# Optimization experiments

Measured on AMD Instinct MI355X. Metric: run time of the kernel, lower is better.

## Reference

```python
import jax, jax.numpy as jnp
import numpy as np

B = 32        # events per batch
NP = 1024     # hits per event (in_hits)
K = 30        # kNN neighbors (includes self, as in PyG knn)
D_IN = 7      # hit feature dim (hardcoded SegmentationNet(7, ...))
OUT = 2       # out_channels


def _edge_conv(x, W1, b1, s, t, W2, b2, k):
    """DynamicEdgeConv: x [B,n,d] -> [B,n,64].
    kNN in feature space, edge MLP on [x_i, x_j - x_i], max-aggregate.
    BN (eval mode) folded into per-channel scale s and shift t."""
    sq = jnp.sum(x * x, axis=-1)                           # [B,n]
    d2 = sq[:, :, None] + sq[:, None, :] - 2.0 * jnp.einsum('bnd,bmd->bnm', x, x)
    _, idx = jax.lax.top_k(-d2, k)                         # [B,n,k] nearest (self included)
    xj = jax.vmap(lambda xb, ib: xb[ib])(x, idx)           # [B,n,k,d] gather neighbors
    xi = jnp.broadcast_to(x[:, :, None, :], xj.shape)
    e = jnp.concatenate([xi, xj - xi], axis=-1)            # [B,n,k,2d]
    h = jax.nn.relu((e @ W1 + b1) * s + t)                 # Linear + BN(eval) + ReLU
    h = h @ W2 + b2                                        # plain last layer (PyG MLP)
    return jnp.max(h, axis=2)                              # max aggregation over k


def setup_inputs() -> dict:
    key = jax.random.key(0)
    ks = jax.random.split(key, 40)
    def lin(k, fi, fo):
        return jax.random.normal(k, (fi, fo), jnp.float32) / np.float32(np.sqrt(fi))
    def vec(k, n, scale=0.1):
        return jax.random.normal(k, (n,), jnp.float32) * np.float32(scale)
    inp = {}
    inp['pos'] = jax.random.normal(ks[0], (B * NP, D_IN), jnp.float32)
    inp['batch'] = jnp.repeat(jnp.arange(B, dtype=jnp.int32), NP)
    inp['batch_size'] = B
    # conv1 edge MLP: [14,64] + BN + ReLU, [64,64]
    inp['c1_W1'] = lin(ks[1], 2 * D_IN, 64); inp['c1_b1'] = vec(ks[2], 64)
    inp['c1_s'] = 1.0 + vec(ks[3], 64); inp['c1_t'] = vec(ks[4], 64)
    inp['c1_W2'] = lin(ks[5], 64, 64); inp['c1_b2'] = vec(ks[6], 64)
    # conv2/conv3: [128,64] + BN + ReLU, [64,64]
    inp['c2_W1'] = lin(ks[7], 128, 64); inp['c2_b1'] = vec(ks[8], 64)
    inp['c2_s'] = 1.0 + vec(ks[9], 64); inp['c2_t'] = vec(ks[10], 64)
    inp['c2_W2'] = lin(ks[11], 64, 64); inp['c2_b2'] = vec(ks[12], 64)
    inp['c3_W1'] = lin(ks[13], 128, 64); inp['c3_b1'] = vec(ks[14], 64)
    inp['c3_s'] = 1.0 + vec(ks[15], 64); inp['c3_t'] = vec(ks[16], 64)
    inp['c3_W2'] = lin(ks[17], 64, 64); inp['c3_b2'] = vec(ks[18], 64)
    # segmentation head MLP [192,1024,256,128,OUT], norm=None, eval (dropout off)
    inp['h_W1'] = lin(ks[19], 192, 1024); inp['h_b1'] = vec(ks[20], 1024)
    inp['h_W2'] = lin(ks[21], 1024, 256); inp['h_b2'] = vec(ks[22], 256)
    inp['h_W3'] = lin(ks[23], 256, 128); inp['h_b3'] = vec(ks[24], 128)
    inp['h_W4'] = lin(ks[25], 128, OUT); inp['h_b4'] = vec(ks[26], OUT)
    # wrapper MLP: Linear(NP*OUT, 100), ReLU, Linear(100, OUT)
    inp['m_W1'] = lin(ks[27], NP * OUT, 100); inp['m_b1'] = vec(ks[28], 100)
    inp['m_W2'] = lin(ks[29], 100, OUT); inp['m_b2'] = vec(ks[30], OUT)
    return inp


def reference(pos, batch, batch_size,
              c1_W1, c1_b1, c1_s, c1_t, c1_W2, c1_b2,
              c2_W1, c2_b1, c2_s, c2_t, c2_W2, c2_b2,
              c3_W1, c3_b1, c3_s, c3_t, c3_W2, c3_b2,
              h_W1, h_b1, h_W2, h_b2, h_W3, h_b3, h_W4, h_b4,
              m_W1, m_b1, m_W2, m_b2):
    n = pos.shape[0] // batch_size
    x = pos.reshape(batch_size, n, -1)          # uniform contiguous graphs per `batch`
    x1 = _edge_conv(x, c1_W1, c1_b1, c1_s, c1_t, c1_W2, c1_b2, K)
    x2 = _edge_conv(x1, c2_W1, c2_b1, c2_s, c2_t, c2_W2, c2_b2, K)
    x3 = _edge_conv(x2, c3_W1, c3_b1, c3_s, c3_t, c3_W2, c3_b2, K)
    h = jnp.concatenate([x1, x2, x3], axis=-1)  # [B,n,192]
    h = jax.nn.relu(h @ h_W1 + h_b1)
    h = jax.nn.relu(h @ h_W2 + h_b2)
    h = jax.nn.relu(h @ h_W3 + h_b3)
    h = h @ h_W4 + h_b4
    seg = jax.nn.log_softmax(h, axis=-1)        # per-node log-probs [B,n,OUT]
    flat = seg.reshape(batch_size, -1)          # [B, n*OUT]
    y = jax.nn.relu(flat @ m_W1 + m_b1) @ m_W2 + m_b2
    return jax.nn.log_softmax(y, axis=-1)       # [B, OUT]
```

## Files before the change

kernel.cpp:

```cpp
#include <hip/hip_runtime.h>
#include <math.h>

#define NPB   1024
#define NB    32
#define NTOT  (NPB * NB)
#define KNN_K 30
#define QB    32
#define DSTR  1028
#define FINF  __builtin_inff()

typedef __attribute__((ext_vector_type(8))) short bf16x8;
typedef __attribute__((ext_vector_type(4))) float f32x4;
typedef unsigned short ushort_t;

__device__ inline ushort_t f2bf(float f) {
  unsigned u = __builtin_bit_cast(unsigned, f);
  u += 0x7FFFu + ((u >> 16) & 1u);
  return (ushort_t)(u >> 16);
}
__device__ inline float bf2f(ushort_t h) {
  return __builtin_bit_cast(float, (unsigned)h << 16);
}

__device__ __forceinline__ void select_row(const float* row, int jbase,
                                           int* out, unsigned* cb, int lane) {
  unsigned u[16];
  #pragma unroll
  for (int i = 0; i < 16; ++i) {
    const unsigned b = __builtin_bit_cast(unsigned, row[lane + (i << 6)]);
    u[i] = b ^ ((unsigned)((int)b >> 31) | 0x80000000u);
  }
  unsigned m = u[0];
  #pragma unroll
  for (int i = 1; i < 16; ++i) m = min(m, u[i]);
  #pragma unroll
  for (int k = 2; k <= 64; k <<= 1) {
    #pragma unroll
    for (int jj = k >> 1; jj >= 1; jj >>= 1) {
      const unsigned o = (unsigned)__shfl_xor((int)m, jj);
      const bool up    = ((lane & k) == 0);
      const bool lower = ((lane & jj) == 0);
      m = (lower == up) ? min(m, o) : max(m, o);
    }
  }
  const unsigned T = (unsigned)__shfl((int)m, 29);

  unsigned mask16 = 0; int cnt = 0;
  #pragma unroll
  for (int i = 0; i < 16; ++i) {
    const bool sv = (u[i] <= T);
    mask16 |= (sv ? 1u : 0u) << i;
    cnt += sv;
  }
  int sc = cnt;
  #pragma unroll
  for (int o = 1; o < 64; o <<= 1) {
    const int v = __shfl_up(sc, o);
    if (lane >= o) sc += v;
  }
  const int base = sc - cnt;
  const int tot  = __shfl(sc, 63);

  if (tot <= 128) {
    int p = base;
    #pragma unroll
    for (int i = 0; i < 16; ++i) {
      if ((mask16 >> i) & 1u)
        cb[p++] = (u[i] & 0xFFFFFC00u) | (unsigned)(lane + (i << 6));
    }
    for (int q = tot + lane; q < 128; q += 64) cb[q] = 0xFFFFFFFFu;
    unsigned r0 = cb[lane];
    unsigned r1 = cb[lane + 64];
    #pragma unroll
    for (int k = 2; k <= 128; k <<= 1) {
      #pragma unroll
      for (int jj = k >> 1; jj >= 1; jj >>= 1) {
        if (jj == 64) {
          const unsigned lo = min(r0, r1), hi = max(r0, r1);
          r0 = lo; r1 = hi;
        } else {
          const unsigned o0 = (unsigned)__shfl_xor((int)r0, jj);
          const unsigned o1 = (unsigned)__shfl_xor((int)r1, jj);
          const bool lower = ((lane & jj) == 0);
          const bool up0 = ((lane & k) == 0);
          const bool up1 = (((lane + 64) & k) == 0);
          r0 = (lower == up0) ? min(r0, o0) : max(r0, o0);
          r1 = (lower == up1) ? min(r1, o1) : max(r1, o1);
        }
      }
    }
    if (lane < KNN_K) out[lane] = jbase + (int)(r0 & 1023u);
  } else {
    unsigned pk[16];
    #pragma unroll
    for (int i = 0; i < 16; ++i)
      pk[i] = (u[i] & 0xFFFFFC00u) | (unsigned)(lane + (i << 6));
    #pragma unroll 1
    for (int k = 0; k < KNN_K; ++k) {
      unsigned best = pk[0];
      #pragma unroll
      for (int i = 1; i < 16; ++i) best = min(best, pk[i]);
      #pragma unroll
      for (int o = 32; o > 0; o >>= 1)
        best = min(best, (unsigned)__shfl_xor((int)best, o));
      if (lane == 0) out[k] = jbase + (int)(best & 1023u);
      #pragma unroll
      for (int i = 0; i < 16; ++i) if (pk[i] == best) pk[i] = 0xFFFFFFFFu;
    }
  }
}

__global__ __launch_bounds__(512)
void knn64_kernel(const ushort_t* __restrict__ X, int lda,
                  const float* __restrict__ sq, int* __restrict__ idx) {
  __shared__ float d2l[QB * DSTR];
  __shared__ float sqa[QB];
  __shared__ unsigned cbuf[8][128];
  const int tid = threadIdx.x;
  const int wave = tid >> 6, lane = tid & 63;
  const int g = lane >> 4, r16 = lane & 15;
  const int nbase = blockIdx.y * NPB;
  const int q0 = blockIdx.x * QB;
  if (tid < QB) sqa[tid] = sq[nbase + q0 + tid];
  __syncthreads();

  const int n0 = wave * 128;
  bf16x8 a0[2], a1[2];
  #pragma unroll
  for (int ks = 0; ks < 2; ++ks) {
    a0[ks] = *(const bf16x8*)(X + (size_t)(nbase + q0 + r16) * lda + ks * 32 + g * 8);
    a1[ks] = *(const bf16x8*)(X + (size_t)(nbase + q0 + 16 + r16) * lda + ks * 32 + g * 8);
  }
  #pragma unroll
  for (int nt = 0; nt < 8; ++nt) {
    const int col = n0 + nt * 16 + r16;
    f32x4 acc0 = (f32x4)(0.f), acc1 = (f32x4)(0.f);
    #pragma unroll
    for (int ks = 0; ks < 2; ++ks) {
      const bf16x8 b = *(const bf16x8*)(X + (size_t)(nbase + col) * lda + ks * 32 + g * 8);
      acc0 = __builtin_amdgcn_mfma_f32_16x16x32_bf16(a0[ks], b, acc0, 0, 0, 0);
      acc1 = __builtin_amdgcn_mfma_f32_16x16x32_bf16(a1[ks], b, acc1, 0, 0, 0);
    }
    const float sb = sq[nbase + col];
    #pragma unroll
    for (int r = 0; r < 4; ++r) {
      const int row0 = g * 4 + r;
      d2l[row0 * DSTR + col] = sqa[row0] + sb - 2.f * acc0[r];
      d2l[(16 + row0) * DSTR + col] = sqa[16 + row0] + sb - 2.f * acc1[r];
    }
  }
  __syncthreads();

  #pragma unroll 1
  for (int rr = 0; rr < 4; ++rr) {
    const int row = wave * 4 + rr;
    select_row(&d2l[row * DSTR], nbase,
               idx + (size_t)(nbase + q0 + row) * KNN_K, cbuf[wave], lane);
  }
}

__global__ __launch_bounds__(512)
void knn7_kernel(const float* __restrict__ pos,
                 const float* __restrict__ sq, int* __restrict__ idx) {
  __shared__ float d2l[QB * DSTR];
  __shared__ float Xq[QB][8];
  __shared__ float sqa[QB];
  __shared__ unsigned cbuf[8][128];
  const int tid = threadIdx.x;
  const int wave = tid >> 6, lane = tid & 63;
  const int nbase = blockIdx.y * NPB;
  const int q0 = blockIdx.x * QB;
  if (tid < QB * 8) {
    const int row = tid >> 3, d = tid & 7;
    Xq[row][d] = (d < 7) ? pos[(size_t)(nbase + q0 + row) * 7 + d] : 0.f;
  }
  if (tid >= 256 && tid < 256 + QB) sqa[tid - 256] = sq[nbase + q0 + tid - 256];
  __syncthreads();

  const int c0 = wave * 128 + lane;
  float xc0[7], xc1[7];
  #pragma unroll
  for (int d = 0; d < 7; ++d) {
    xc0[d] = pos[(size_t)(nbase + c0) * 7 + d];
    xc1[d] = pos[(size_t)(nbase + c0 + 64) * 7 + d];
  }
  const float sb0 = sq[nbase + c0], sb1 = sq[nbase + c0 + 64];
  #pragma unroll 1
  for (int row = 0; row < QB; ++row) {
    float q[7];
    #pragma unroll
    for (int d = 0; d < 7; ++d) q[d] = Xq[row][d];
    float d0 = 0.f, d1 = 0.f;
    #pragma unroll
    for (int d = 0; d < 7; ++d) { d0 += q[d] * xc0[d]; d1 += q[d] * xc1[d]; }
    const float sa = sqa[row];
    d2l[row * DSTR + c0]      = sa + sb0 - 2.f * d0;
    d2l[row * DSTR + c0 + 64] = sa + sb1 - 2.f * d1;
  }
  __syncthreads();

  #pragma unroll 1
  for (int rr = 0; rr < 4; ++rr) {
    const int row = wave * 4 + rr;
    select_row(&d2l[row * DSTR], nbase,
               idx + (size_t)(nbase + q0 + row) * KNN_K, cbuf[wave], lane);
  }
}

template<int D>
__global__ __launch_bounds__(256)
void sq_kernel(const float* __restrict__ x, int lda, float* __restrict__ sq) {
  const int wave = threadIdx.x >> 6, c = threadIdx.x & 63;
  const int nb = blockIdx.x * 16 + wave * 4;
  #pragma unroll
  for (int i = 0; i < 4; ++i) {
    const float xv = (c < D) ? x[(size_t)(nb + i) * lda + c] : 0.f;
    float p = xv * xv;
    #pragma unroll
    for (int o = 32; o > 0; o >>= 1) p += __shfl_down(p, o);
    if (c == 0) sq[nb + i] = p;
  }
}
__global__ __launch_bounds__(256)
void sqbf_kernel(const ushort_t* __restrict__ x, int lda, float* __restrict__ sq) {
  const int wave = threadIdx.x >> 6, c = threadIdx.x & 63;
  const int nb = blockIdx.x * 16 + wave * 4;
  #pragma unroll
  for (int i = 0; i < 4; ++i) {
    const float xv = bf2f(x[(size_t)(nb + i) * lda + c]);
    float p = xv * xv;
    #pragma unroll
    for (int o = 32; o > 0; o >>= 1) p += __shfl_down(p, o);
    if (c == 0) sq[nb + i] = p;
  }
}

__global__ __launch_bounds__(256)
void wprep_kernel(const float* __restrict__ W1, const float* __restrict__ b1,
                  const float* __restrict__ s, const float* __restrict__ t,
                  int D, ushort_t* __restrict__ BTc, float* __restrict__ biasc) {
  const int i = blockIdx.x * 256 + threadIdx.x;
  if (i >= 128 * 64) return;
  const int n = i >> 6, k = i & 63;
  float v = 0.f;
  if (k < D) {
    if (n < 64) v = (W1[k * 64 + n] - W1[(D + k) * 64 + n]) * s[n];
    else        v = W1[(D + k) * 64 + (n - 64)] * s[n - 64];
  }
  BTc[i] = f2bf(v);
  if (k == 0) biasc[n] = (n < 64) ? (b1[n] * s[n] + t[n]) : 0.f;
}

__global__ __launch_bounds__(256)
void pospad_kernel(const float* __restrict__ pos, ushort_t* __restrict__ xpad) {
  const int i = blockIdx.x * 256 + threadIdx.x;
  const int node = i >> 6, k = i & 63;
  xpad[i] = f2bf(k < 7 ? pos[(size_t)node * 7 + k] : 0.f);
}

__global__ __launch_bounds__(256)
void wcvt_kernel(const float* __restrict__ W, ushort_t* __restrict__ BT,
                 int K, int N) {
  const int i = blockIdx.x * 256 + threadIdx.x;
  if (i >= N * K) return;
  const int n = i / K, k = i % K;
  BT[i] = f2bf(W[(size_t)k * N + n]);
}

__global__ __launch_bounds__(256)
void edge_mfma_kernel(const ushort_t* __restrict__ av,
                      const int* __restrict__ idx,
                      const ushort_t* __restrict__ W2T, const float* __restrict__ b2,
                      ushort_t* __restrict__ xbf) {
  const int lane = threadIdx.x & 63;
  const int wave = threadIdx.x >> 6;
  const int g = lane >> 4, r16 = lane & 15;
  const int node0 = blockIdx.x * 16 + wave * 4;

  bf16x8 bf[2][4];
  #pragma unroll
  for (int ks = 0; ks < 2; ++ks)
    #pragma unroll
    for (int nt = 0; nt < 4; ++nt)
      bf[ks][nt] = *(const bf16x8*)(W2T + (nt * 16 + r16) * 64 + ks * 32 + g * 8);

  const float b2c = b2[lane];

  #pragma unroll 1
  for (int nn = 0; nn < 4; ++nn) {
    const int node = node0 + nn;
    float asf[2][8];
    {
      const ushort_t* ar = av + (size_t)node * 128;
      #pragma unroll
      for (int ks = 0; ks < 2; ++ks) {
        union { uint4 v; ushort_t s[8]; } u;
        u.v = *(const uint4*)(ar + ks * 32 + g * 8);
        #pragma unroll
        for (int i = 0; i < 8; ++i) asf[ks][i] = bf2f(u.s[i]);
      }
    }
    const int j0 = idx[(size_t)node * KNN_K + r16];
    const int e1 = 16 + r16;
    const int j1 = idx[(size_t)node * KNN_K + (e1 < KNN_K ? e1 : KNN_K - 1)];

    f32x4 acc[2][4];
    #pragma unroll
    for (int mt = 0; mt < 2; ++mt)
      #pragma unroll
      for (int nt = 0; nt < 4; ++nt) acc[mt][nt] = (f32x4)(0.f);

    #pragma unroll
    for (int mt = 0; mt < 2; ++mt) {
      const int j = mt ? j1 : j0;
      const ushort_t* vr = av + (size_t)j * 128 + 64;
      #pragma unroll
      for (int ks = 0; ks < 2; ++ks) {
        union { uint4 v; ushort_t s[8]; } u;
        u.v = *(const uint4*)(vr + ks * 32 + g * 8);
        bf16x8 af;
        #pragma unroll
        for (int i = 0; i < 8; ++i) {
          const float hh = fmaxf(asf[ks][i] + bf2f(u.s[i]), 0.f);
          af[i] = (short)f2bf(hh);
        }
        #pragma unroll
        for (int nt = 0; nt < 4; ++nt)
          acc[mt][nt] = __builtin_amdgcn_mfma_f32_16x16x32_bf16(af, bf[ks][nt], acc[mt][nt], 0, 0, 0);
      }
    }

    float cm[4];
    #pragma unroll
    for (int nt = 0; nt < 4; ++nt) {
      float m0 = fmaxf(fmaxf(acc[0][nt][0], acc[0][nt][1]), fmaxf(acc[0][nt][2], acc[0][nt][3]));
      float m1 = fmaxf(fmaxf(acc[1][nt][0], acc[1][nt][1]), fmaxf(acc[1][nt][2], acc[1][nt][3]));
      float m = fmaxf(m0, m1);
      m = fmaxf(m, __shfl_xor(m, 16));
      m = fmaxf(m, __shfl_xor(m, 32));
      cm[nt] = m;
    }
    const float v = (g == 0) ? cm[0] : (g == 1) ? cm[1] : (g == 2) ? cm[2] : cm[3];
    xbf[(size_t)node * 192 + lane] = f2bf(v + b2c);
  }
}

template<bool RELU, typename CT>
__global__ __launch_bounds__(256)
void gemm_bf16_kernel(const ushort_t* __restrict__ A, int lda,
                      const ushort_t* __restrict__ BT, int ldb,
                      const float* __restrict__ bias,
                      CT* __restrict__ C, int ldc, int K) {
  __shared__ ushort_t As[128 * 72];
  __shared__ ushort_t Bs[128 * 72];
  const int tid = threadIdx.x;
  const int lane = tid & 63;
  const int g = lane >> 4, r16 = lane & 15;
  const int wv = tid >> 6, wm = wv >> 1, wn = wv & 1;
  const int bm = blockIdx.x * 128, bn = blockIdx.y * 128;

  f32x4 acc[4][4];
  #pragma unroll
  for (int mt = 0; mt < 4; ++mt)
    #pragma unroll
    for (int nt = 0; nt < 4; ++nt) acc[mt][nt] = (f32x4)(0.f);

  const int srow = tid >> 1, scq = (tid & 1) * 32;
  for (int k0 = 0; k0 < K; k0 += 64) {
    const ushort_t* ap = A + (size_t)(bm + srow) * lda + k0 + scq;
    const ushort_t* bp = BT + (size_t)(bn + srow) * ldb + k0 + scq;
    uint4 av0 = *(const uint4*)(ap);      uint4 av1 = *(const uint4*)(ap + 8);
    uint4 av2 = *(const uint4*)(ap + 16); uint4 av3 = *(const uint4*)(ap + 24);
    uint4 bv0 = *(const uint4*)(bp);      uint4 bv1 = *(const uint4*)(bp + 8);
    uint4 bv2 = *(const uint4*)(bp + 16); uint4 bv3 = *(const uint4*)(bp + 24);
    __syncthreads();
    *(uint4*)(As + srow * 72 + scq +  0) = av0;
    *(uint4*)(As + srow * 72 + scq +  8) = av1;
    *(uint4*)(As + srow * 72 + scq + 16) = av2;
    *(uint4*)(As + srow * 72 + scq + 24) = av3;
    *(uint4*)(Bs + srow * 72 + scq +  0) = bv0;
    *(uint4*)(Bs + srow * 72 + scq +  8) = bv1;
    *(uint4*)(Bs + srow * 72 + scq + 16) = bv2;
    *(uint4*)(Bs + srow * 72 + scq + 24) = bv3;
    __syncthreads();
    #pragma unroll
    for (int ks = 0; ks < 2; ++ks) {
      bf16x8 a[4], b[4];
      #pragma unroll
      for (int mt = 0; mt < 4; ++mt)
        a[mt] = *(const bf16x8*)(As + (wm * 64 + mt * 16 + r16) * 72 + ks * 32 + g * 8);
      #pragma unroll
      for (int nt = 0; nt < 4; ++nt)
        b[nt] = *(const bf16x8*)(Bs + (wn * 64 + nt * 16 + r16) * 72 + ks * 32 + g * 8);
      #pragma unroll
      for (int mt = 0; mt < 4; ++mt)
        #pragma unroll
        for (int nt = 0; nt < 4; ++nt)
          acc[mt][nt] = __builtin_amdgcn_mfma_f32_16x16x32_bf16(a[mt], b[nt], acc[mt][nt], 0, 0, 0);
    }
  }

  #pragma unroll
  for (int nt = 0; nt < 4; ++nt) {
    const int col = bn + wn * 64 + nt * 16 + r16;
    const float bv = bias[col];
    #pragma unroll
    for (int mt = 0; mt < 4; ++mt) {
      #pragma unroll
      for (int r = 0; r < 4; ++r) {
        const int row = bm + wm * 64 + mt * 16 + g * 4 + r;
        float val = acc[mt][nt][r] + bv;
        if (RELU) val = fmaxf(val, 0.f);
        if constexpr (sizeof(CT) == 2) C[(size_t)row * ldc + col] = f2bf(val);
        else                           C[(size_t)row * ldc + col] = val;
      }
    }
  }
}

__global__ __launch_bounds__(256)
void g4_kernel(const ushort_t* __restrict__ h3, const float* __restrict__ W4,
               const float* __restrict__ b4, float* __restrict__ seg) {
  const int row = blockIdx.x * 4 + (threadIdx.x >> 6);
  const int lane = threadIdx.x & 63;
  const ushort_t* hr = h3 + (size_t)row * 128;
  float p0 = 0.f, p1 = 0.f;
  #pragma unroll
  for (int h = 0; h < 2; ++h) {
    const int r = lane + h * 64;
    const float hv = bf2f(hr[r]);
    p0 += hv * W4[r * 2 + 0];
    p1 += hv * W4[r * 2 + 1];
  }
  #pragma unroll
  for (int o = 32; o > 0; o >>= 1) { p0 += __shfl_down(p0, o); p1 += __shfl_down(p1, o); }
  if (lane == 0) {
    const float l0 = p0 + b4[0], l1 = p1 + b4[1];
    const float mx = fmaxf(l0, l1);
    const float lse = mx + logf(expf(l0 - mx) + expf(l1 - mx));
    seg[(size_t)row * 2 + 0] = l0 - lse;
    seg[(size_t)row * 2 + 1] = l1 - lse;
  }
}

__global__ __launch_bounds__(256)
void wrapper_kernel(const float* __restrict__ seg, const float* __restrict__ W1,
                    const float* __restrict__ b1, const float* __restrict__ W2,
                    const float* __restrict__ b2, float* __restrict__ out) {
  __shared__ float fl[NPB * 2];
  __shared__ float part[2][128];
  __shared__ float y1[100];
  __shared__ float l2[2];
  const int b = blockIdx.x, tid = threadIdx.x;
  for (int i = tid; i < NPB * 2; i += 256) fl[i] = seg[(size_t)b * NPB * 2 + i];
  __syncthreads();
  {
    const int c = tid & 127, p = tid >> 7;
    float acc = 0.f;
    if (c < 100) {
      const int r0 = p * (NPB);
      #pragma unroll 16
      for (int r = 0; r < NPB; ++r)
        acc += fl[r0 + r] * W1[(size_t)(r0 + r) * 100 + c];
    }
    part[p][c] = acc;
  }
  __syncthreads();
  if (tid < 100) {
    y1[tid] = fmaxf(part[0][tid] + part[1][tid] + b1[tid], 0.f);
  }
  __syncthreads();
  if (tid < 2) {
    float acc = b2[tid];
    for (int j = 0; j < 100; ++j) acc += y1[j] * W2[j * 2 + tid];
    l2[tid] = acc;
  }
  __syncthreads();
  if (tid == 0) {
    const float l0 = l2[0], l1 = l2[1];
    const float mx = fmaxf(l0, l1);
    const float lse = mx + logf(expf(l0 - mx) + expf(l1 - mx));
    out[b * 2 + 0] = l0 - lse;
    out[b * 2 + 1] = l1 - lse;
  }
}

extern "C" void kernel_launch(void* const* d_in, const int* in_sizes, int n_in,
                              void* d_out, int out_size, void* d_ws, size_t ws_size,
                              hipStream_t stream) {
  const float* pos   = (const float*)d_in[0];
  const float* c1_W1 = (const float*)d_in[3];
  const float* c1_b1 = (const float*)d_in[4];
  const float* c1_s  = (const float*)d_in[5];
  const float* c1_t  = (const float*)d_in[6];
  const float* c1_W2 = (const float*)d_in[7];
  const float* c1_b2 = (const float*)d_in[8];
  const float* c2_W1 = (const float*)d_in[9];
  const float* c2_b1 = (const float*)d_in[10];
  const float* c2_s  = (const float*)d_in[11];
  const float* c2_t  = (const float*)d_in[12];
  const float* c2_W2 = (const float*)d_in[13];
  const float* c2_b2 = (const float*)d_in[14];
  const float* c3_W1 = (const float*)d_in[15];
  const float* c3_b1 = (const float*)d_in[16];
  const float* c3_s  = (const float*)d_in[17];
  const float* c3_t  = (const float*)d_in[18];
  const float* c3_W2 = (const float*)d_in[19];
  const float* c3_b2 = (const float*)d_in[20];
  const float* h_W1  = (const float*)d_in[21];
  const float* h_b1  = (const float*)d_in[22];
  const float* h_W2  = (const float*)d_in[23];
  const float* h_b2  = (const float*)d_in[24];
  const float* h_W3  = (const float*)d_in[25];
  const float* h_b3  = (const float*)d_in[26];
  const float* h_W4  = (const float*)d_in[27];
  const float* h_b4  = (const float*)d_in[28];
  const float* m_W1  = (const float*)d_in[29];
  const float* m_b1  = (const float*)d_in[30];
  const float* m_W2  = (const float*)d_in[31];
  const float* m_b2  = (const float*)d_in[32];

  float* ws = (float*)d_ws;
  size_t off = 0;
  auto alloc = [&](size_t n) {
    float* p = ws + off;
    off += (n + 63) & ~(size_t)63;
    return p;
  };
  ushort_t* xbf   = (ushort_t*)alloc((size_t)NTOT * 96);
  int*      idx   = (int*)alloc((size_t)NTOT * KNN_K);
  ushort_t* avbuf = (ushort_t*)alloc((size_t)NTOT * 64);
  ushort_t* xpad  = (ushort_t*)alloc((size_t)NTOT * 32);
  float*    sqb   = alloc(NTOT);
  float*    seg   = alloc((size_t)NTOT * 2);
  ushort_t* BT1   = (ushort_t*)alloc(1024 * 192 / 2);
  ushort_t* BT2   = (ushort_t*)alloc(256 * 1024 / 2);
  ushort_t* BT3   = (ushort_t*)alloc(128 * 256 / 2);
  ushort_t* BTc1  = (ushort_t*)alloc(128 * 64 / 2);
  ushort_t* BTc2  = (ushort_t*)alloc(128 * 64 / 2);
  ushort_t* BTc3  = (ushort_t*)alloc(128 * 64 / 2);
  ushort_t* W2T1  = (ushort_t*)alloc(64 * 64 / 2);
  ushort_t* W2T2  = (ushort_t*)alloc(64 * 64 / 2);
  ushort_t* W2T3  = (ushort_t*)alloc(64 * 64 / 2);
  float*    bc1   = alloc(128);
  float*    bc2   = alloc(128);
  float*    bc3   = alloc(128);

  const size_t totf = ws_size / 4;
  const size_t avail = (totf > off + 1024) ? (totf - off - 1024) : 0;
  int CH = 1;
  while (CH < 256 && (size_t)(NTOT / CH) * 704 > avail) CH <<= 1;
  const int CR = NTOT / CH;
  ushort_t* h1 = (ushort_t*)(ws + off);
  ushort_t* h2 = h1 + (size_t)CR * 1024;
  ushort_t* h3 = h2 + (size_t)CR * 256;

  wcvt_kernel<<<(192 * 1024 + 255) / 256, 256, 0, stream>>>(h_W1, BT1, 192, 1024);
  wcvt_kernel<<<(1024 * 256 + 255) / 256, 256, 0, stream>>>(h_W2, BT2, 1024, 256);
  wcvt_kernel<<<(256 * 128 + 255) / 256, 256, 0, stream>>>(h_W3, BT3, 256, 128);
  wcvt_kernel<<<16, 256, 0, stream>>>(c1_W2, W2T1, 64, 64);
  wcvt_kernel<<<16, 256, 0, stream>>>(c2_W2, W2T2, 64, 64);
  wcvt_kernel<<<16, 256, 0, stream>>>(c3_W2, W2T3, 64, 64);
  wprep_kernel<<<32, 256, 0, stream>>>(c1_W1, c1_b1, c1_s, c1_t, 7,  BTc1, bc1);
  wprep_kernel<<<32, 256, 0, stream>>>(c2_W1, c2_b1, c2_s, c2_t, 64, BTc2, bc2);
  wprep_kernel<<<32, 256, 0, stream>>>(c3_W1, c3_b1, c3_s, c3_t, 64, BTc3, bc3);
  pospad_kernel<<<NTOT * 64 / 256, 256, 0, stream>>>(pos, xpad);

  auto run_av = [&](const ushort_t* A, int lda, const ushort_t* BTc, const float* bc) {
    gemm_bf16_kernel<false, ushort_t><<<dim3(NTOT / 128, 1), 256, 0, stream>>>(
        A, lda, BTc, 64, bc, avbuf, 128, 64);
  };

  sq_kernel<7><<<NTOT / 16, 256, 0, stream>>>(pos, 7, sqb);
  run_av(xpad, 64, BTc1, bc1);
  knn7_kernel<<<dim3(NPB / QB, NB), 512, 0, stream>>>(pos, sqb, idx);
  edge_mfma_kernel<<<NTOT / 16, 256, 0, stream>>>(avbuf, idx, W2T1, c1_b2, xbf + 0);

  sqbf_kernel<<<NTOT / 16, 256, 0, stream>>>(xbf + 0, 192, sqb);
  run_av(xbf + 0, 192, BTc2, bc2);
  knn64_kernel<<<dim3(NPB / QB, NB), 512, 0, stream>>>(xbf + 0, 192, sqb, idx);
  edge_mfma_kernel<<<NTOT / 16, 256, 0, stream>>>(avbuf, idx, W2T2, c2_b2, xbf + 64);

  sqbf_kernel<<<NTOT / 16, 256, 0, stream>>>(xbf + 64, 192, sqb);
  run_av(xbf + 64, 192, BTc3, bc3);
  knn64_kernel<<<dim3(NPB / QB, NB), 512, 0, stream>>>(xbf + 64, 192, sqb, idx);
  edge_mfma_kernel<<<NTOT / 16, 256, 0, stream>>>(avbuf, idx, W2T3, c3_b2, xbf + 128);

  for (int ch = 0; ch < CH; ++ch) {
    const ushort_t* Ax = xbf + (size_t)ch * CR * 192;
    gemm_bf16_kernel<true, ushort_t><<<dim3(CR / 128, 8), 256, 0, stream>>>(Ax, 192, BT1, 192, h_b1, h1, 1024, 192);
    gemm_bf16_kernel<true, ushort_t><<<dim3(CR / 128, 2), 256, 0, stream>>>(h1, 1024, BT2, 1024, h_b2, h2, 256, 1024);
    gemm_bf16_kernel<true, ushort_t><<<dim3(CR / 128, 1), 256, 0, stream>>>(h2, 256, BT3, 256, h_b3, h3, 128, 256);
    g4_kernel<<<CR / 4, 256, 0, stream>>>(h3, h_W4, h_b4, seg + (size_t)ch * CR * 2);
  }

  wrapper_kernel<<<NB, 256, 0, stream>>>(seg, m_W1, m_b1, m_W2, m_b2, (float*)d_out);
}
```

Before: 468.9 us.

## Halve kNN query block and pack distance keys when writing to LDS

Reduces the kNN query tile from 32 to 16 rows, so each block does one MFMA tile per column group and each wave selects 2 rows instead of 4. This halves the per-block LDS distance buffer, letting more blocks fit on a CU. Distances are also converted to order-preserving keys with the column index packed in as they are written, so the selection routine no longer re-packs them. The cost is twice as many blocks, each reloading the full 1024-column operand and its squared norms.

```diff
diff --git a/kernel.cpp b/kernel.cpp
--- a/kernel.cpp
+++ b/kernel.cpp
@@ -5,7 +5,7 @@
 #define NB    32
 #define NTOT  (NPB * NB)
 #define KNN_K 30
-#define QB    32
+#define QB    16
 #define DSTR  1028
 #define FINF  __builtin_inff()
 
@@ -21,15 +21,18 @@
 __device__ inline float bf2f(ushort_t h) {
   return __builtin_bit_cast(float, (unsigned)h << 16);
 }
-
-__device__ __forceinline__ void select_row(const float* row, int jbase,
-                                           int* out, unsigned* cb, int lane) {
+__device__ inline unsigned packkey(float d, int col) {
+  unsigned u = __builtin_bit_cast(unsigned, d);
+  u ^= ((unsigned)((int)u >> 31) | 0x80000000u);
+  return (u & 0xFFFFFC00u) | (unsigned)col;
+}
+
+__device__ __forceinline__ void select_row_packed(const unsigned* row, int jbase,
+                                                  int* out, unsigned* cb, int lane) {
   unsigned u[16];
   #pragma unroll
-  for (int i = 0; i < 16; ++i) {
-    const unsigned b = __builtin_bit_cast(unsigned, row[lane + (i << 6)]);
-    u[i] = b ^ ((unsigned)((int)b >> 31) | 0x80000000u);
-  }
+  for (int i = 0; i < 16; ++i) u[i] = row[lane + (i << 6)];
+
   unsigned m = u[0];
   #pragma unroll
   for (int i = 1; i < 16; ++i) m = min(m, u[i]);
@@ -65,8 +68,7 @@
     int p = base;
     #pragma unroll
     for (int i = 0; i < 16; ++i) {
-      if ((mask16 >> i) & 1u)
-        cb[p++] = (u[i] & 0xFFFFFC00u) | (unsigned)(lane + (i << 6));
+      if ((mask16 >> i) & 1u) cb[p++] = u[i];
     }
     for (int q = tot + lane; q < 128; q += 64) cb[q] = 0xFFFFFFFFu;
     unsigned r0 = cb[lane];
@@ -93,8 +95,7 @@
   } else {
     unsigned pk[16];
     #pragma unroll
-    for (int i = 0; i < 16; ++i)
-      pk[i] = (u[i] & 0xFFFFFC00u) | (unsigned)(lane + (i << 6));
+    for (int i = 0; i < 16; ++i) pk[i] = u[i];
     #pragma unroll 1
     for (int k = 0; k < KNN_K; ++k) {
       unsigned best = pk[0];
@@ -113,7 +114,7 @@
 __global__ __launch_bounds__(512)
 void knn64_kernel(const ushort_t* __restrict__ X, int lda,
                   const float* __restrict__ sq, int* __restrict__ idx) {
-  __shared__ float d2l[QB * DSTR];
+  __shared__ unsigned d2l[QB * DSTR];
   __shared__ float sqa[QB];
   __shared__ unsigned cbuf[8][128];
   const int tid = threadIdx.x;
@@ -125,44 +126,41 @@
   __syncthreads();
 
   const int n0 = wave * 128;
-  bf16x8 a0[2], a1[2];
-  #pragma unroll
-  for (int ks = 0; ks < 2; ++ks) {
+  bf16x8 a0[2];
+  #pragma unroll
+  for (int ks = 0; ks < 2; ++ks)
     a0[ks] = *(const bf16x8*)(X + (size_t)(nbase + q0 + r16) * lda + ks * 32 + g * 8);
-    a1[ks] = *(const bf16x8*)(X + (size_t)(nbase + q0 + 16 + r16) * lda + ks * 32 + g * 8);
-  }
+
   #pragma unroll
   for (int nt = 0; nt < 8; ++nt) {
     const int col = n0 + nt * 16 + r16;
-    f32x4 acc0 = (f32x4)(0.f), acc1 = (f32x4)(0.f);
+    f32x4 acc0 = (f32x4)(0.f);
     #pragma unroll
     for (int ks = 0; ks < 2; ++ks) {
       const bf16x8 b = *(const bf16x8*)(X + (size_t)(nbase + col) * lda + ks * 32 + g * 8);
       acc0 = __builtin_amdgcn_mfma_f32_16x16x32_bf16(a0[ks], b, acc0, 0, 0, 0);
-      acc1 = __builtin_amdgcn_mfma_f32_16x16x32_bf16(a1[ks], b, acc1, 0, 0, 0);
     }
     const float sb = sq[nbase + col];
     #pragma unroll
     for (int r = 0; r < 4; ++r) {
       const int row0 = g * 4 + r;
-      d2l[row0 * DSTR + col] = sqa[row0] + sb - 2.f * acc0[r];
-      d2l[(16 + row0) * DSTR + col] = sqa[16 + row0] + sb - 2.f * acc1[r];
+      d2l[row0 * DSTR + col] = packkey(sqa[row0] + sb - 2.f * acc0[r], col);
     }
   }
   __syncthreads();
 
   #pragma unroll 1
-  for (int rr = 0; rr < 4; ++rr) {
-    const int row = wave * 4 + rr;
-    select_row(&d2l[row * DSTR], nbase,
-               idx + (size_t)(nbase + q0 + row) * KNN_K, cbuf[wave], lane);
+  for (int rr = 0; rr < 2; ++rr) {
+    const int row = wave * 2 + rr;
+    select_row_packed(&d2l[row * DSTR], nbase,
+                      idx + (size_t)(nbase + q0 + row) * KNN_K, cbuf[wave], lane);
   }
 }
 
 __global__ __launch_bounds__(512)
 void knn7_kernel(const float* __restrict__ pos,
                  const float* __restrict__ sq, int* __restrict__ idx) {
-  __shared__ float d2l[QB * DSTR];
+  __shared__ unsigned d2l[QB * DSTR];
   __shared__ float Xq[QB][8];
   __shared__ float sqa[QB];
   __shared__ unsigned cbuf[8][128];
@@ -194,16 +192,16 @@
     #pragma unroll
     for (int d = 0; d < 7; ++d) { d0 += q[d] * xc0[d]; d1 += q[d] * xc1[d]; }
     const float sa = sqa[row];
-    d2l[row * DSTR + c0]      = sa + sb0 - 2.f * d0;
-    d2l[row * DSTR + c0 + 64] = sa + sb1 - 2.f * d1;
+    d2l[row * DSTR + c0]      = packkey(sa + sb0 - 2.f * d0, c0);
+    d2l[row * DSTR + c0 + 64] = packkey(sa + sb1 - 2.f * d1, c0 + 64);
   }
   __syncthreads();
 
   #pragma unroll 1
-  for (int rr = 0; rr < 4; ++rr) {
-    const int row = wave * 4 + rr;
-    select_row(&d2l[row * DSTR], nbase,
-               idx + (size_t)(nbase + q0 + row) * KNN_K, cbuf[wave], lane);
+  for (int rr = 0; rr < 2; ++rr) {
+    const int row = wave * 2 + rr;
+    select_row_packed(&d2l[row * DSTR], nbase,
+                      idx + (size_t)(nbase + q0 + row) * KNN_K, cbuf[wave], lane);
   }
 }
 
```

Result: faster. 414.1 us (-11.7%).
